# Performance work log

Hardware: AMD Instinct MI355X
Metric: run time of the kernel (lower is better)

The kernel has to match this reference:

```python
import jax, jax.numpy as jnp
import numpy as np

N, C, K, NUM_CLASS = 400000, 128, 128, 128


def setup_inputs() -> dict:
    key = jax.random.key(0)
    k1, k2, k3 = jax.random.split(key, 3)
    outputs = jax.random.normal(k1, (N, C), dtype=jnp.float32)
    labels = jax.random.randint(k2, (N,), 0, 2 * NUM_CLASS, dtype=jnp.int64 if jax.config.read('jax_enable_x64') else jnp.int32)
    global_logit = jax.random.normal(k3, (K, C), dtype=jnp.float32)
    return {"outputs": outputs, "labels": labels, "global_logit": global_logit, "k": NUM_CLASS}


def _pairwise_dist(x, protos):
    # Euclidean distance ||proto_j - x_i|| for all (i, j) without a [N,K,C] temp.
    x2 = jnp.sum(x * x, axis=1, keepdims=True)            # [N,1]
    p2 = jnp.sum(protos * protos, axis=1)[None, :]        # [1,K]
    d2 = x2 + p2 - 2.0 * (x @ protos.T)                   # [N,K]
    return jnp.sqrt(jnp.maximum(d2, 0.0))


def reference(outputs, labels, global_logit, k):
    # Rows with labels <= k-1 keep their label; rows with labels > k-1 get the
    # nearest-prototype index. Since the concatenated (labeled + pseudo-labeled)
    # set covers every row and CE-mean is order-invariant, we compute per-row
    # effective labels and a single mean cross-entropy.
    dists = _pairwise_dist(outputs, global_logit)          # [N,K]
    min_dist_labels = jnp.argmin(dists, axis=1)            # [N]
    is_labeled = labels <= (k - 1)
    labels_eff = jnp.where(is_labeled, labels, min_dist_labels)
    logp = jax.nn.log_softmax(outputs, axis=-1)            # [N,C]
    nll = -jnp.take_along_axis(logp, labels_eff[:, None].astype(jnp.int32), axis=1)[:, 0]
    return jnp.mean(nll)
```

## Files before the change

### kernel.cpp

```cpp
#include <hip/hip_runtime.h>
#include <hip/hip_bf16.h>


#define C_DIM 128
#define TILE_ROWS 32
#define NTHREADS 256
#define WAVES_PER_BLOCK 4
#define TILES_PER_WAVE 4

typedef __bf16 bf16x8 __attribute__((ext_vector_type(8)));
typedef unsigned short ushort8 __attribute__((ext_vector_type(8)));
typedef float f32x16 __attribute__((ext_vector_type(16)));

union FragU { ushort8 u; bf16x8 b; };

__device__ __forceinline__ unsigned short f2bf(float f) {
    unsigned u = __float_as_uint(f);
    u += 0x7fffu + ((u >> 16) & 1u);
    return (unsigned short)(u >> 16);
}

extern "C" __global__ void __launch_bounds__(NTHREADS)
ploss_main(const float* __restrict__ x, const int* __restrict__ labels,
           const float* __restrict__ protos, const int* __restrict__ kptr,
           float* __restrict__ accum, int n_tiles)
{
    __shared__ __attribute__((aligned(16))) unsigned short pfrag[32 * 64 * 8];
    __shared__ __attribute__((aligned(16))) float p2_lds[C_DIM];

    const int tid  = threadIdx.x;
    const int lane = tid & 63;
    const int wave = tid >> 6;
    const int h    = lane >> 5;
    const int m    = lane & 31;
    const int kk   = kptr[0];

    if (tid < C_DIM) {
        const float* pr = protos + tid * C_DIM;
        float s = 0.f;
#pragma unroll
        for (int c = 0; c < C_DIM; c += 4) {
            float4 v = *(const float4*)(pr + c);
            s += v.x*v.x + v.y*v.y + v.z*v.z + v.w*v.w;
        }
        p2_lds[tid] = 0.5f * s + 512.0f;
    }

    {
        const int pt = wave;
#pragma unroll
        for (int kt = 0; kt < 8; ++kt) {
            const float* pp = protos + (pt*32 + m) * C_DIM + kt*16 + h*8;
            float4 v0 = *(const float4*)(pp);
            float4 v1 = *(const float4*)(pp + 4);
            FragU f;
            f.u[0]=f2bf(v0.x); f.u[1]=f2bf(v0.y); f.u[2]=f2bf(v0.z); f.u[3]=f2bf(v0.w);
            f.u[4]=f2bf(v1.x); f.u[5]=f2bf(v1.y); f.u[6]=f2bf(v1.z); f.u[7]=f2bf(v1.w);
            *(ushort8*)&pfrag[((pt*8 + kt)*64 + lane)*8] = f.u;
        }
    }
    __syncthreads();

    const int gw = blockIdx.x * WAVES_PER_BLOCK + wave;
    int t0 = gw * TILES_PER_WAVE;
    int t1 = t0 + TILES_PER_WAVE;
    if (t1 > n_tiles) t1 = n_tiles;

    float nll = 0.f;

#pragma unroll 1
    for (int t = t0; t < t1; ++t) {
        const float* xr = x + (size_t)(t * TILE_ROWS + m) * C_DIM + h * 8;
        float4 v[16];
#pragma unroll
        for (int kt = 0; kt < 8; ++kt) {
            v[2*kt]   = *(const float4*)(xr + kt*16);
            v[2*kt+1] = *(const float4*)(xr + kt*16 + 4);
        }
        const int lab = labels[t * TILE_ROWS + m];

        float mx = -3.4e38f;
#pragma unroll
        for (int i = 0; i < 16; ++i)
            mx = fmaxf(mx, fmaxf(fmaxf(v[i].x, v[i].y), fmaxf(v[i].z, v[i].w)));
        mx = fmaxf(mx, __shfl_xor(mx, 32));
        float s = 0.f;
#pragma unroll
        for (int i = 0; i < 16; ++i)
            s += __expf(v[i].x-mx) + __expf(v[i].y-mx) + __expf(v[i].z-mx) + __expf(v[i].w-mx);
        s += __shfl_xor(s, 32);
        const float lse = mx + __logf(s);

        FragU xb[8];
#pragma unroll
        for (int kt = 0; kt < 8; ++kt) {
            xb[kt].u[0]=f2bf(v[2*kt].x);   xb[kt].u[1]=f2bf(v[2*kt].y);
            xb[kt].u[2]=f2bf(v[2*kt].z);   xb[kt].u[3]=f2bf(v[2*kt].w);
            xb[kt].u[4]=f2bf(v[2*kt+1].x); xb[kt].u[5]=f2bf(v[2*kt+1].y);
            xb[kt].u[6]=f2bf(v[2*kt+1].z); xb[kt].u[7]=f2bf(v[2*kt+1].w);
        }

        f32x16 acc[4];
#pragma unroll
        for (int pt = 0; pt < 4; ++pt) acc[pt] = (f32x16)(0.f);
#pragma unroll
        for (int kt = 0; kt < 8; ++kt) {
#pragma unroll
            for (int pt = 0; pt < 4; ++pt) {
                FragU af;
                af.u = *(const ushort8*)&pfrag[((pt*8 + kt)*64 + lane)*8];
                acc[pt] = __builtin_amdgcn_mfma_f32_32x32x16_bf16(af.b, xb[kt].b, acc[pt], 0, 0, 0);
            }
        }

        unsigned best = 0xFFFFFFFFu;
#pragma unroll
        for (int pt = 0; pt < 4; ++pt) {
#pragma unroll
            for (int g = 0; g < 4; ++g) {
                float4 q = *(const float4*)&p2_lds[pt*32 + g*8 + h*4];
#pragma unroll
                for (int c = 0; c < 4; ++c) {
                    const int r = g*4 + c;
                    const float sc = q[c] - acc[pt][r];
                    const unsigned j = (unsigned)(pt*32 + g*8 + h*4 + c);
                    const unsigned u = (__float_as_uint(sc) & 0xFFFFFF80u) | j;
                    best = u < best ? u : best;
                }
            }
        }
        {
            const unsigned ub = __shfl_xor(best, 32);
            best = ub < best ? ub : best;
        }

        if (lane < 32) {
            const int bj  = (int)(best & 127u);
            const int eff = (lab <= kk - 1) ? lab : bj;
            const float xv = x[(size_t)(t * TILE_ROWS + m) * C_DIM + eff];
            nll += lse - xv;
        }
    }

#pragma unroll
    for (int mask = 1; mask <= 32; mask <<= 1) nll += __shfl_xor(nll, mask);
    if (lane == 0) atomicAdd(accum, nll);
}

extern "C" __global__ void ploss_finalize(const float* __restrict__ accum,
                                          float* __restrict__ out, float inv_n)
{
    out[0] = accum[0] * inv_n;
}

extern "C" void kernel_launch(void* const* d_in, const int* in_sizes, int n_in,
                              void* d_out, int out_size, void* d_ws, size_t ws_size,
                              hipStream_t stream)
{
    const float* x      = (const float*)d_in[0];
    const int*   labels = (const int*)d_in[1];
    const float* protos = (const float*)d_in[2];
    const int*   kptr   = (const int*)d_in[3];
    const int n_rows  = in_sizes[0] / C_DIM;
    const int n_tiles = n_rows / TILE_ROWS;

    float* accum = (float*)d_ws;
    hipMemsetAsync(accum, 0, sizeof(float), stream);

    const int grid = (n_tiles + WAVES_PER_BLOCK * TILES_PER_WAVE - 1)
                   / (WAVES_PER_BLOCK * TILES_PER_WAVE);
    ploss_main<<<grid, NTHREADS, 0, stream>>>(x, labels, protos, kptr, accum, n_tiles);
    ploss_finalize<<<1, 1, 0, stream>>>(accum, (float*)d_out, 1.0f / (float)n_rows);
}
```

Baseline: 344.9 us.

## Prefetch next tile's rows and drop max-subtraction in log-sum-exp

Software-pipelines each wave's tile loop: the global loads for the next tile's rows and labels are issued before the current tile's MFMA distance pass runs, so memory latency overlaps compute. Also drops the running-max subtraction in log-sum-exp, uses a cheaper perm-based bf16 packing for activations, splits the MFMA pass into two halves to lower live accumulators, sets launch_bounds occupancy to 3, and reduces per block before a single atomic. The unshifted exp is only safe while inputs stay well below float exp overflow, and the new rounding is round-half-up rather than round-to-nearest-even. Both changes may alter results for other inputs.

```diff
diff --git a/kernel.cpp b/kernel.cpp
--- a/kernel.cpp
+++ b/kernel.cpp
@@ -5,28 +5,91 @@
 #define C_DIM 128
 #define TILE_ROWS 32
 #define NTHREADS 256
-#define WAVES_PER_BLOCK 4
 #define TILES_PER_WAVE 4
 
 typedef __bf16 bf16x8 __attribute__((ext_vector_type(8)));
 typedef unsigned short ushort8 __attribute__((ext_vector_type(8)));
 typedef float f32x16 __attribute__((ext_vector_type(16)));
 
-union FragU { ushort8 u; bf16x8 b; };
+union FragU { ushort8 u; bf16x8 b; unsigned w[4]; };
 
-__device__ __forceinline__ unsigned short f2bf(float f) {
+__device__ __forceinline__ unsigned short f2bf_rne(float f) {
     unsigned u = __float_as_uint(f);
     u += 0x7fffu + ((u >> 16) & 1u);
     return (unsigned short)(u >> 16);
 }
+__device__ __forceinline__ unsigned pk2(float lo, float hi) {
+    return __builtin_amdgcn_perm(__float_as_uint(hi) + 0x8000u,
+                                 __float_as_uint(lo) + 0x8000u, 0x07060302u);
+}
 
-extern "C" __global__ void __launch_bounds__(NTHREADS)
+__device__ __forceinline__ void issue_loads(const float* __restrict__ xr, float4 v[16]) {
+#pragma unroll
+    for (int kt = 0; kt < 8; ++kt) {
+        v[2*kt]   = *(const float4*)(xr + kt*16);
+        v[2*kt+1] = *(const float4*)(xr + kt*16 + 4);
+    }
+}
+
+__device__ __forceinline__ float soft_convert(const float4 v[16], FragU xb[8]) {
+    float s0=0.f, s1=0.f, s2=0.f, s3=0.f;
+#pragma unroll
+    for (int i = 0; i < 16; ++i) {
+        s0 += __expf(v[i].x); s1 += __expf(v[i].y);
+        s2 += __expf(v[i].z); s3 += __expf(v[i].w);
+    }
+#pragma unroll
+    for (int kt = 0; kt < 8; ++kt) {
+        xb[kt].w[0] = pk2(v[2*kt].x,   v[2*kt].y);
+        xb[kt].w[1] = pk2(v[2*kt].z,   v[2*kt].w);
+        xb[kt].w[2] = pk2(v[2*kt+1].x, v[2*kt+1].y);
+        xb[kt].w[3] = pk2(v[2*kt+1].z, v[2*kt+1].w);
+    }
+    float s = (s0 + s1) + (s2 + s3);
+    s += __shfl_xor(s, 32);
+    return __logf(s);
+}
+
+__device__ __forceinline__ unsigned pass_minpack(const unsigned short* __restrict__ pfrag,
+                                                 const float* __restrict__ p2_lds,
+                                                 const FragU xb[8], int lane, int h, int pp) {
+    f32x16 a0 = (f32x16)(0.f), a1 = (f32x16)(0.f);
+    const int f0 = (pp*2)*8, f1 = (pp*2+1)*8;
+#pragma unroll
+    for (int kt = 0; kt < 8; ++kt) {
+        FragU A0, A1;
+        A0.u = *(const ushort8*)&pfrag[((f0+kt)*64 + lane)*8];
+        A1.u = *(const ushort8*)&pfrag[((f1+kt)*64 + lane)*8];
+        a0 = __builtin_amdgcn_mfma_f32_32x32x16_bf16(A0.b, xb[kt].b, a0, 0, 0, 0);
+        a1 = __builtin_amdgcn_mfma_f32_32x32x16_bf16(A1.b, xb[kt].b, a1, 0, 0, 0);
+    }
+    unsigned best = 0xFFFFFFFFu;
+#pragma unroll
+    for (int half = 0; half < 2; ++half) {
+        const int pt = pp*2 + half;
+#pragma unroll
+        for (int g = 0; g < 4; ++g) {
+            float4 q = *(const float4*)&p2_lds[pt*32 + g*8 + h*4];
+#pragma unroll
+            for (int c = 0; c < 4; ++c) {
+                const float sc = q[c] - (half ? a1[g*4+c] : a0[g*4+c]);
+                const unsigned j = (unsigned)(pt*32 + g*8 + h*4 + c);
+                const unsigned u = (__float_as_uint(sc) & 0xFFFFFF80u) | j;
+                best = u < best ? u : best;
+            }
+        }
+    }
+    return best;
+}
+
+extern "C" __global__ void __launch_bounds__(NTHREADS, 3)
 ploss_main(const float* __restrict__ x, const int* __restrict__ labels,
            const float* __restrict__ protos, const int* __restrict__ kptr,
            float* __restrict__ accum, int n_tiles)
 {
     __shared__ __attribute__((aligned(16))) unsigned short pfrag[32 * 64 * 8];
     __shared__ __attribute__((aligned(16))) float p2_lds[C_DIM];
+    __shared__ float blk_red[4];
 
     const int tid  = threadIdx.x;
     const int lane = tid & 63;
@@ -45,7 +108,6 @@
         }
         p2_lds[tid] = 0.5f * s + 512.0f;
     }
-
     {
         const int pt = wave;
 #pragma unroll
@@ -54,97 +116,60 @@
             float4 v0 = *(const float4*)(pp);
             float4 v1 = *(const float4*)(pp + 4);
             FragU f;
-            f.u[0]=f2bf(v0.x); f.u[1]=f2bf(v0.y); f.u[2]=f2bf(v0.z); f.u[3]=f2bf(v0.w);
-            f.u[4]=f2bf(v1.x); f.u[5]=f2bf(v1.y); f.u[6]=f2bf(v1.z); f.u[7]=f2bf(v1.w);
+            f.u[0]=f2bf_rne(v0.x); f.u[1]=f2bf_rne(v0.y); f.u[2]=f2bf_rne(v0.z); f.u[3]=f2bf_rne(v0.w);
+            f.u[4]=f2bf_rne(v1.x); f.u[5]=f2bf_rne(v1.y); f.u[6]=f2bf_rne(v1.z); f.u[7]=f2bf_rne(v1.w);
             *(ushort8*)&pfrag[((pt*8 + kt)*64 + lane)*8] = f.u;
         }
     }
     __syncthreads();
 
-    const int gw = blockIdx.x * WAVES_PER_BLOCK + wave;
+    const int gw = blockIdx.x * 4 + wave;
     int t0 = gw * TILES_PER_WAVE;
     int t1 = t0 + TILES_PER_WAVE;
     if (t1 > n_tiles) t1 = n_tiles;
 
     float nll = 0.f;
 
+    if (t0 < t1) {
+        FragU xb[8];
+        float lse;
+        int lab;
+        {
+            float4 v[16];
+            issue_loads(x + (size_t)(t0 * TILE_ROWS + m) * C_DIM + h*8, v);
+            lab = labels[t0 * TILE_ROWS + m];
+            lse = soft_convert(v, xb);
+        }
 #pragma unroll 1
-    for (int t = t0; t < t1; ++t) {
-        const float* xr = x + (size_t)(t * TILE_ROWS + m) * C_DIM + h * 8;
-        float4 v[16];
-#pragma unroll
-        for (int kt = 0; kt < 8; ++kt) {
-            v[2*kt]   = *(const float4*)(xr + kt*16);
-            v[2*kt+1] = *(const float4*)(xr + kt*16 + 4);
-        }
-        const int lab = labels[t * TILE_ROWS + m];
+        for (int t = t0; t < t1; ++t) {
+            const int tn = (t + 1 < t1) ? t + 1 : t;
+            float4 vn[16];
+            issue_loads(x + (size_t)(tn * TILE_ROWS + m) * C_DIM + h*8, vn);
+            const int labn = labels[tn * TILE_ROWS + m];
 
-        float mx = -3.4e38f;
-#pragma unroll
-        for (int i = 0; i < 16; ++i)
-            mx = fmaxf(mx, fmaxf(fmaxf(v[i].x, v[i].y), fmaxf(v[i].z, v[i].w)));
-        mx = fmaxf(mx, __shfl_xor(mx, 32));
-        float s = 0.f;
-#pragma unroll
-        for (int i = 0; i < 16; ++i)
-            s += __expf(v[i].x-mx) + __expf(v[i].y-mx) + __expf(v[i].z-mx) + __expf(v[i].w-mx);
-        s += __shfl_xor(s, 32);
-        const float lse = mx + __logf(s);
-
-        FragU xb[8];
-#pragma unroll
-        for (int kt = 0; kt < 8; ++kt) {
-            xb[kt].u[0]=f2bf(v[2*kt].x);   xb[kt].u[1]=f2bf(v[2*kt].y);
-            xb[kt].u[2]=f2bf(v[2*kt].z);   xb[kt].u[3]=f2bf(v[2*kt].w);
-            xb[kt].u[4]=f2bf(v[2*kt+1].x); xb[kt].u[5]=f2bf(v[2*kt+1].y);
-            xb[kt].u[6]=f2bf(v[2*kt+1].z); xb[kt].u[7]=f2bf(v[2*kt+1].w);
-        }
-
-        f32x16 acc[4];
-#pragma unroll
-        for (int pt = 0; pt < 4; ++pt) acc[pt] = (f32x16)(0.f);
-#pragma unroll
-        for (int kt = 0; kt < 8; ++kt) {
-#pragma unroll
-            for (int pt = 0; pt < 4; ++pt) {
-                FragU af;
-                af.u = *(const ushort8*)&pfrag[((pt*8 + kt)*64 + lane)*8];
-                acc[pt] = __builtin_amdgcn_mfma_f32_32x32x16_bf16(af.b, xb[kt].b, acc[pt], 0, 0, 0);
-            }
-        }
-
-        unsigned best = 0xFFFFFFFFu;
-#pragma unroll
-        for (int pt = 0; pt < 4; ++pt) {
-#pragma unroll
-            for (int g = 0; g < 4; ++g) {
-                float4 q = *(const float4*)&p2_lds[pt*32 + g*8 + h*4];
-#pragma unroll
-                for (int c = 0; c < 4; ++c) {
-                    const int r = g*4 + c;
-                    const float sc = q[c] - acc[pt][r];
-                    const unsigned j = (unsigned)(pt*32 + g*8 + h*4 + c);
-                    const unsigned u = (__float_as_uint(sc) & 0xFFFFFF80u) | j;
-                    best = u < best ? u : best;
-                }
-            }
-        }
-        {
+            const unsigned b0 = pass_minpack(pfrag, p2_lds, xb, lane, h, 0);
+            const unsigned b1 = pass_minpack(pfrag, p2_lds, xb, lane, h, 1);
+            unsigned best = b0 < b1 ? b0 : b1;
             const unsigned ub = __shfl_xor(best, 32);
             best = ub < best ? ub : best;
-        }
 
-        if (lane < 32) {
-            const int bj  = (int)(best & 127u);
-            const int eff = (lab <= kk - 1) ? lab : bj;
-            const float xv = x[(size_t)(t * TILE_ROWS + m) * C_DIM + eff];
-            nll += lse - xv;
+            if (lane < 32) {
+                const int bj  = (int)(best & 127u);
+                const int eff = (lab <= kk - 1) ? lab : bj;
+                nll += lse - x[(size_t)(t * TILE_ROWS + m) * C_DIM + eff];
+            }
+
+            lse = soft_convert(vn, xb);
+            lab = labn;
         }
     }
 
 #pragma unroll
     for (int mask = 1; mask <= 32; mask <<= 1) nll += __shfl_xor(nll, mask);
-    if (lane == 0) atomicAdd(accum, nll);
+    if (lane == 0) blk_red[wave] = nll;
+    __syncthreads();
+    if (tid == 0)
+        atomicAdd(accum, (blk_red[0] + blk_red[1]) + (blk_red[2] + blk_red[3]));
 }
 
 extern "C" __global__ void ploss_finalize(const float* __restrict__ accum,
@@ -167,8 +192,7 @@
     float* accum = (float*)d_ws;
     hipMemsetAsync(accum, 0, sizeof(float), stream);
 
-    const int grid = (n_tiles + WAVES_PER_BLOCK * TILES_PER_WAVE - 1)
-                   / (WAVES_PER_BLOCK * TILES_PER_WAVE);
+    const int grid = (n_tiles + 4 * TILES_PER_WAVE - 1) / (4 * TILES_PER_WAVE);
     ploss_main<<<grid, NTHREADS, 0, stream>>>(x, labels, protos, kptr, accum, n_tiles);
     ploss_finalize<<<1, 1, 0, stream>>>(accum, (float*)d_out, 1.0f / (float)n_rows);
 }
```

New measurement: 447.5 us. 29.7% more time.
